# Kernel optimization log

Hardware: AMD Instinct MI355X
Metric: run time of the kernel (lower is better)

The kernel has to match this reference:

```python
import jax, jax.numpy as jnp
import numpy as np

NSAMPLE = 32
EPS = 1e-5


def _fps(xyz, npoint):
    # xyz: [B, N, 3] -> indices [B, npoint] (farthest point sampling, start at idx 0)
    B, N, _ = xyz.shape
    def body(i, state):
        idx, dist, far = state
        idx = idx.at[:, i].set(far)
        centroid = jnp.take_along_axis(xyz, far[:, None, None], axis=1)  # [B,1,3]
        d = jnp.sum((xyz - centroid) ** 2, axis=-1)                      # [B,N]
        dist = jnp.minimum(dist, d)
        far = jnp.argmax(dist, axis=-1).astype(jnp.int32)
        return idx, dist, far
    idx0 = jnp.zeros((B, npoint), jnp.int32)
    dist0 = jnp.full((B, N), 1e10, xyz.dtype)
    far0 = jnp.zeros((B,), jnp.int32)
    idx, _, _ = jax.lax.fori_loop(0, npoint, body, (idx0, dist0, far0))
    return idx


def _knn(query, ref, k):
    # query [B,S,3], ref [B,N,3] -> neighbor idx [B,S,k]
    d = (jnp.sum(query * query, -1)[:, :, None]
         - 2.0 * jnp.einsum('bsc,bnc->bsn', query, ref)
         + jnp.sum(ref * ref, -1)[:, None, :])
    _, idx = jax.lax.top_k(-d, k)
    return idx


def _gather(x, idx):
    # x [B,N,C], idx [B,S,K] -> [B,S,K,C]
    B, S, K = idx.shape
    out = jnp.take_along_axis(x, idx.reshape(B, S * K)[..., None], axis=1)
    return out.reshape(B, S, K, x.shape[-1])


def _set_abstraction(xyz, feat, npoint, weights):
    # xyz [B,N,3], feat [B,N,C]
    fidx = _fps(xyz, npoint)
    new_xyz = jnp.take_along_axis(xyz, fidx[..., None], axis=1)        # [B,S,3]
    nidx = _knn(new_xyz, xyz, NSAMPLE)                                 # [B,S,K]
    g_xyz = _gather(xyz, nidx) - new_xyz[:, :, None, :]                # [B,S,K,3]
    g_feat = _gather(feat, nidx)                                       # [B,S,K,C]
    x = jnp.concatenate([g_xyz, g_feat], axis=-1)                      # [B,S,K,3+C]
    for W in weights:  # 1x1 conv == per-point matmul, then InstanceNorm2d (affine=False) + ReLU
        x = jnp.einsum('bskc,cd->bskd', x, W)
        mu = jnp.mean(x, axis=(1, 2), keepdims=True)
        var = jnp.var(x, axis=(1, 2), keepdims=True)
        x = jax.nn.relu((x - mu) * jax.lax.rsqrt(var + EPS))
    new_feat = jnp.max(x, axis=2)                                      # [B,S,Cout]
    return new_xyz, new_feat, fidx


def setup_inputs() -> dict:
    key = jax.random.key(0)
    ks = jax.random.split(key, 8)
    B, N = 4, 16384
    pc = jax.random.normal(ks[0], (B, 3, N), jnp.float32)
    feature = jax.random.normal(ks[1], (B, 3, N), jnp.float32)
    def w(k, cin, cout):
        return jax.random.normal(k, (cin, cout), jnp.float32) / np.sqrt(cin).astype(np.float32)
    return {
        'pc': pc, 'feature': feature,
        'sa1_w1': w(ks[2], 6, 32),  'sa1_w2': w(ks[3], 32, 32), 'sa1_w3': w(ks[4], 32, 32),
        'sa2_w1': w(ks[5], 35, 64), 'sa2_w2': w(ks[6], 64, 64), 'sa2_w3': w(ks[7], 64, 64),
    }


def reference(pc, feature, sa1_w1, sa1_w2, sa1_w3, sa2_w1, sa2_w2, sa2_w3):
    NPOINT = 4096
    xyz = jnp.transpose(pc, (0, 2, 1))       # [B,N,3]
    feat = jnp.transpose(feature, (0, 2, 1))  # [B,N,3]
    xyz1, feat1, fidx1 = _set_abstraction(xyz, feat, NPOINT // 2, [sa1_w1, sa1_w2, sa1_w3])
    xyz2, feat2, fidx2 = _set_abstraction(xyz1, feat1, NPOINT // 4, [sa2_w1, sa2_w2, sa2_w3])
    # match torch channel-first layout on outputs
    pc_l1 = jnp.transpose(xyz1, (0, 2, 1))
    pc_l2 = jnp.transpose(xyz2, (0, 2, 1))
    feat_l2 = jnp.transpose(feat2, (0, 2, 1))  # [B,64,NPOINT//4]
    return (pc, pc_l1, pc_l2, feat_l2, fidx1, fidx2)
```

## Files before the change

kernel.cpp:

```cpp
#include <hip/hip_runtime.h>
#include <math.h>

namespace {

constexpr int BB = 4;
constexpr int N0 = 16384;
constexpr int S1 = 2048;
constexpr int S2 = 1024;

__device__ __forceinline__ float sq3(float x, float y, float z){
  #pragma clang fp contract(off)
  return x*x + y*y + z*z;
}
__device__ __forceinline__ float sqdist(float ax,float ay,float az,float bx,float by,float bz){
  #pragma clang fp contract(off)
  float dx = ax-bx; float dy = ay-by; float dz = az-bz;
  return dx*dx + dy*dy + dz*dz;
}
__device__ __forceinline__ float dot3(float ax,float ay,float az,float bx,float by,float bz){
  #pragma clang fp contract(off)
  return ax*bx + ay*by + az*bz;
}
__device__ __forceinline__ float knndist(float qs, float dot, float rs){
  #pragma clang fp contract(off)
  return (qs - 2.0f*dot) + rs;
}

__global__ __launch_bounds__(256) void k_setup(const float* __restrict__ pc,
                                               const float* __restrict__ feat,
                                               float* __restrict__ out_pc,
                                               float* __restrict__ xyz,
                                               float* __restrict__ fN,
                                               float* __restrict__ rsq0)
{
  int t = blockIdx.x*256 + threadIdx.x;
  if (t < BB*3*N0) out_pc[t] = pc[t];
  if (t < BB*N0){
    int b = t >> 14, n = t & (N0-1);
    const float* p = pc + (size_t)b*3*N0;
    float x = p[n], y = p[N0+n], z = p[2*N0+n];
    float* q = xyz + (size_t)t*3;
    q[0]=x; q[1]=y; q[2]=z;
    rsq0[t] = sq3(x,y,z);
    const float* f = feat + (size_t)b*3*N0;
    float* g = fN + (size_t)t*3;
    g[0]=f[n]; g[1]=f[N0+n]; g[2]=f[2*N0+n];
  }
}

__device__ __forceinline__ void fps_writeout(int b, int i, float cx, float cy, float cz, int far,
                                             float* sxyz, float* srsq, float* pcl, float* fidxf, int NP)
{
  fidxf[(size_t)b*NP + i] = (float)far;
  float* o = sxyz + ((size_t)b*NP + i)*3;
  o[0]=cx; o[1]=cy; o[2]=cz;
  float* pb = pcl + (size_t)b*3*NP;
  pb[i] = cx; pb[NP+i] = cy; pb[2*NP+i] = cz;
  srsq[(size_t)b*NP + i] = sq3(cx,cy,cz);
}

template<int N, int NP, int BS, int PPT>
__device__ __forceinline__ void fps_body(const float* __restrict__ pts,
                                         float* __restrict__ sxyz,
                                         float* __restrict__ srsq,
                                         float* __restrict__ pcl,
                                         float* __restrict__ fidxf)
{
  static_assert(N == BS*PPT, "bad fps shape");
  constexpr int NW = BS/64;
  int b = blockIdx.x, t = threadIdx.x;
  int lane = t & 63;
  int wid  = t >> 6;
  const float* P = pts + (size_t)b*N*3;

  __shared__ unsigned long long slot[2][NW];

  float px[PPT], py[PPT], pz[PPT], dist[PPT];
  #pragma unroll
  for (int j=0;j<PPT;j++){
    int g = t + BS*j;
    px[j]=P[g*3]; py[j]=P[g*3+1]; pz[j]=P[g*3+2];
    asm volatile("" : "+v"(px[j]), "+v"(py[j]), "+v"(pz[j]));
    dist[j]=1e10f;
  }

  float cx = P[0], cy = P[1], cz = P[2];
  if (t == 0) fps_writeout(b, 0, cx, cy, cz, 0, sxyz, srsq, pcl, fidxf, NP);

  for (int i=1;i<NP;i++){
    int par = i & 1;
    float msq = -1.0f;
    #pragma unroll
    for (int j=0;j<PPT;j++){
      float d  = sqdist(px[j],py[j],pz[j],cx,cy,cz);
      float nd = fminf(dist[j], d);
      dist[j]  = nd;
      msq = fmaxf(msq, nd);
    }
    #pragma unroll
    for (int off=32; off>0; off>>=1) msq = fmaxf(msq, __shfl_xor(msq, off));
    float s = sqrtf(msq);
    unsigned xb = __float_as_uint(msq);
    while (xb > 0u && sqrtf(__uint_as_float(xb - 1u)) == s) xb--;
    float lo = __uint_as_float(xb);
    int li = 0x7FFFFFFF;
    #pragma unroll
    for (int j=PPT-1;j>=0;j--) if (dist[j] >= lo) li = t + BS*j;
    #pragma unroll
    for (int off=32; off>0; off>>=1) li = min(li, __shfl_xor(li, off));
    if (lane == 0)
      slot[par][wid] = ((unsigned long long)__float_as_uint(s) << 32)
                     | (unsigned long long)(unsigned)(~li);
    __syncthreads();
    unsigned long long best = slot[par][0];
    #pragma unroll
    for (int w=1; w<NW; w++){
      unsigned long long o = slot[par][w];
      best = (o > best) ? o : best;
    }
    int far = (int)(~(unsigned)best);
    far = __builtin_amdgcn_readfirstlane(far);
    cx = P[(size_t)far*3]; cy = P[(size_t)far*3+1]; cz = P[(size_t)far*3+2];
    if (t == 0) fps_writeout(b, i, cx, cy, cz, far, sxyz, srsq, pcl, fidxf, NP);
  }
}

__global__ __attribute__((amdgpu_flat_work_group_size(512,512), amdgpu_waves_per_eu(2,2)))
void k_fps1(const float* __restrict__ pts, float* __restrict__ sxyz, float* __restrict__ srsq,
            float* __restrict__ pcl, float* __restrict__ fidxf)
{
  fps_body<N0, S1, 512, 32>(pts, sxyz, srsq, pcl, fidxf);
}

__global__ __attribute__((amdgpu_flat_work_group_size(512,512), amdgpu_waves_per_eu(2,2)))
void k_fps2(const float* __restrict__ pts, float* __restrict__ sxyz, float* __restrict__ srsq,
            float* __restrict__ pcl, float* __restrict__ fidxf)
{
  fps_body<S1, S2, 512, 4>(pts, sxyz, srsq, pcl, fidxf);
}

template<int NREF, int PPT, int NQ>
__global__ __launch_bounds__(512) void k_knn(const float* __restrict__ qxyz,
                                             const float* __restrict__ qrsq,
                                             const float* __restrict__ rxyz,
                                             const float* __restrict__ rrsq,
                                             int* __restrict__ nidx)
{
  static_assert(NREF == 512*PPT, "bad knn shape");
  int q = blockIdx.x;
  int b = q / NQ;
  int t = threadIdx.x;
  const float* R  = rxyz + (size_t)b*NREF*3;
  const float* RS = rrsq + (size_t)b*NREF;
  float qx = qxyz[(size_t)q*3], qy = qxyz[(size_t)q*3+1], qz = qxyz[(size_t)q*3+2];
  float qs = qrsq[q];
  unsigned u[PPT];
  #pragma unroll
  for (int j=0;j<PPT;j++){
    int g = t + 512*j;
    float rx=R[g*3], ry=R[g*3+1], rz=R[g*3+2];
    float d = knndist(qs, dot3(qx,qy,qz,rx,ry,rz), RS[g]);
    unsigned bu = __float_as_uint(d);
    u[j] = ((int)bu < 0) ? ~bu : (bu | 0x80000000u);
  }
  __shared__ unsigned hist[256];
  __shared__ unsigned s_pref, s_pm, s_want, s_cnteq;
  __shared__ int s_n;
  __shared__ int s_eq[1024];
  __shared__ int s_ne;
  if (t == 0){ s_pref=0u; s_pm=0u; s_want=32u; s_n=0; s_ne=0; }

  for (int shift=24; shift>=0; shift-=8){
    if (t < 256) hist[t] = 0u;
    __syncthreads();
    unsigned pref = s_pref, pm = s_pm;
    #pragma unroll
    for (int j=0;j<PPT;j++){
      if ((u[j] & pm) == pref) atomicAdd(&hist[(u[j]>>shift)&255], 1u);
    }
    __syncthreads();
    if (t < 64){
      unsigned h0=hist[4*t], h1=hist[4*t+1], h2=hist[4*t+2], h3=hist[4*t+3];
      unsigned ssum = h0+h1+h2+h3;
      unsigned inc = ssum;
      #pragma unroll
      for (int off=1; off<64; off<<=1){
        unsigned o = __shfl_up(inc, off);
        if (t >= off) inc += o;
      }
      unsigned exc = inc - ssum;
      unsigned want = s_want;
      if (exc < want && want <= inc){
        unsigned rem = want - exc;
        unsigned bin, below;
        if      (rem <= h0)       { bin=4*t+0; below=exc; }
        else if (rem <= h0+h1)    { bin=4*t+1; below=exc+h0; }
        else if (rem <= h0+h1+h2) { bin=4*t+2; below=exc+h0+h1; }
        else                      { bin=4*t+3; below=exc+h0+h1+h2; }
        s_pref = pref | (bin << shift);
        s_pm   = pm   | (0xFFu << shift);
        s_want = want - below;
        if (shift == 0) s_cnteq = hist[bin];
      }
    }
    __syncthreads();
  }
  unsigned T = s_pref;
  unsigned krem = s_want;
  unsigned cnteq = s_cnteq;
  int* outq = nidx + (size_t)q*32;
  #pragma unroll
  for (int j=0;j<PPT;j++){
    if (u[j] < T){ int p = atomicAdd(&s_n, 1); outq[p] = t + 512*j; }
  }
  __syncthreads();
  if (cnteq == krem){
    #pragma unroll
    for (int j=0;j<PPT;j++){
      if (u[j] == T){ int p = atomicAdd(&s_n, 1); outq[p] = t + 512*j; }
    }
  } else {
    #pragma unroll
    for (int j=0;j<PPT;j++){
      if (u[j] == T){ int p = atomicAdd(&s_ne, 1); if (p < 1024) s_eq[p] = t + 512*j; }
    }
    __syncthreads();
    if (t == 0){
      int ne = s_ne; if (ne > 1024) ne = 1024;
      int p = s_n;
      int take = (int)krem; if (take > ne) take = ne;
      for (int r=0; r<take; r++){
        int mn = 0x7FFFFFFF, mi = -1;
        for (int e=0; e<ne; e++){ if (s_eq[e] < mn){ mn = s_eq[e]; mi = e; } }
        if (mi < 0) break;
        outq[p++] = mn;
        s_eq[mi] = 0x7FFFFFFF;
      }
    }
  }
}

template<int C>
__device__ __forceinline__ void accum_sums(const float* o, int b, float* sums){
  __shared__ float s_sum[C];
  __shared__ float s_ssq[C];
  int t = threadIdx.x;
  if (t < C){ s_sum[t]=0.f; s_ssq[t]=0.f; }
  __syncthreads();
  int lane = t & 63;
  #pragma unroll
  for (int c=0;c<C;c++){
    float v = o[c], v2 = v*v;
    #pragma unroll
    for (int off=32; off>0; off>>=1){ v += __shfl_down(v, off); v2 += __shfl_down(v2, off); }
    if (lane == 0){ atomicAdd(&s_sum[c], v); atomicAdd(&s_ssq[c], v2); }
  }
  __syncthreads();
  if (t < C){
    atomicAdd(&sums[(b*64+t)*2],   s_sum[t]);
    atomicAdd(&sums[(b*64+t)*2+1], s_ssq[t]);
  }
}

__global__ __launch_bounds__(256) void k_sa1_l1(const float* __restrict__ xyz,
                                                const float* __restrict__ fN,
                                                const float* __restrict__ sxyz,
                                                const int* __restrict__ nidx,
                                                const float* __restrict__ W,
                                                float* __restrict__ xout,
                                                float* __restrict__ sums)
{
  __shared__ float sW[192];
  int t = threadIdx.x;
  if (t < 192) sW[t] = W[t];
  int row = blockIdx.x*256 + t;
  int b = row >> 16;
  int sk = row & 65535;
  int s = sk >> 5;
  int nb = nidx[row];
  const float* pr = xyz  + ((size_t)(b*N0 + nb))*3;
  const float* pq = sxyz + ((size_t)(b*S1 + s ))*3;
  const float* pf = fN   + ((size_t)(b*N0 + nb))*3;
  float i0 = pr[0]-pq[0], i1 = pr[1]-pq[1], i2 = pr[2]-pq[2];
  float i3 = pf[0], i4 = pf[1], i5 = pf[2];
  __syncthreads();
  float o[32];
  #pragma unroll
  for (int c=0;c<32;c++){
    float a = i0*sW[c];
    a = fmaf(i1, sW[ 32+c], a);
    a = fmaf(i2, sW[ 64+c], a);
    a = fmaf(i3, sW[ 96+c], a);
    a = fmaf(i4, sW[128+c], a);
    a = fmaf(i5, sW[160+c], a);
    o[c] = a;
    xout[(size_t)c*262144 + row] = a;
  }
  accum_sums<32>(o, b, sums);
}

template<int CIN, int COUT, int LRPB>
__global__ __launch_bounds__(256) void k_sa_mid(const float* __restrict__ xin,
                                                const float* __restrict__ W,
                                                const float* __restrict__ sums_in,
                                                float* __restrict__ xout,
                                                float* __restrict__ sums_out,
                                                int rows_total, float invM)
{
  __shared__ float sW[CIN*COUT];
  __shared__ float s_mu[CIN];
  __shared__ float s_rs[CIN];
  int t = threadIdx.x;
  int row = blockIdx.x*256 + t;
  int bb = (blockIdx.x*256) >> LRPB;
  for (int i=t; i<CIN*COUT; i+=256) sW[i] = W[i];
  if (t < CIN){
    float sm = sums_in[(bb*64+t)*2], sq = sums_in[(bb*64+t)*2+1];
    float mu = sm*invM;
    float var = fmaxf(sq*invM - mu*mu, 0.f);
    s_mu[t] = mu;
    s_rs[t] = 1.0f/sqrtf(var + 1e-5f);
  }
  __syncthreads();
  float o[COUT];
  #pragma unroll
  for (int d=0;d<COUT;d++) o[d] = 0.f;
  #pragma unroll
  for (int c=0;c<CIN;c++){
    float x = xin[(size_t)c*rows_total + row];
    float v = fmaxf((x - s_mu[c])*s_rs[c], 0.f);
    #pragma unroll
    for (int d=0;d<COUT;d++) o[d] = fmaf(v, sW[c*COUT+d], o[d]);
  }
  #pragma unroll
  for (int d=0;d<COUT;d++) xout[(size_t)d*rows_total + row] = o[d];
  accum_sums<COUT>(o, bb, sums_out);
}

__global__ __launch_bounds__(256) void k_sa2_l1(const float* __restrict__ xyz1,
                                                const float* __restrict__ feat1,
                                                const float* __restrict__ xyz2,
                                                const int* __restrict__ nidx,
                                                const float* __restrict__ W,
                                                float* __restrict__ xout,
                                                float* __restrict__ sums)
{
  __shared__ float sW[35*64];
  int t = threadIdx.x;
  for (int i=t; i<35*64; i+=256) sW[i] = W[i];
  int row = blockIdx.x*256 + t;
  int b = row >> 15;
  int sk = row & 32767;
  int s = sk >> 5;
  int nb = nidx[row];
  const float* pr = xyz1 + ((size_t)(b*S1 + nb))*3;
  const float* pq = xyz2 + ((size_t)(b*S2 + s ))*3;
  const float* pf = feat1 + ((size_t)(b*S1 + nb))*32;
  float i0 = pr[0]-pq[0], i1 = pr[1]-pq[1], i2 = pr[2]-pq[2];
  float fv[32];
  #pragma unroll
  for (int c=0;c<32;c++) fv[c] = pf[c];
  __syncthreads();
  float o[64];
  #pragma unroll
  for (int d=0;d<64;d++){
    float a = i0*sW[d];
    a = fmaf(i1, sW[ 64+d], a);
    a = fmaf(i2, sW[128+d], a);
    o[d] = a;
  }
  #pragma unroll
  for (int c=0;c<32;c++){
    float v = fv[c];
    #pragma unroll
    for (int d=0;d<64;d++) o[d] = fmaf(v, sW[(3+c)*64+d], o[d]);
  }
  #pragma unroll
  for (int d=0;d<64;d++) xout[(size_t)d*131072 + row] = o[d];
  accum_sums<64>(o, b, sums);
}

template<int C, int PTSB, int CF>
__global__ __launch_bounds__(256) void k_pool(const float* __restrict__ xin,
                                              const float* __restrict__ sums_in,
                                              float* __restrict__ out,
                                              int rows_total, float invM)
{
  int t = threadIdx.x;
  int c = t & (C-1);
  int pl = t / C;
  int p = blockIdx.x*(256/C) + pl;
  int b = p / PTSB;
  float sm = sums_in[(b*64+c)*2], sq = sums_in[(b*64+c)*2+1];
  float mu = sm*invM;
  float var = fmaxf(sq*invM - mu*mu, 0.f);
  float rs = 1.0f/sqrtf(var + 1e-5f);
  const float* xp = xin + (size_t)c*rows_total + (size_t)p*32;
  float m = -1e30f;
  #pragma unroll
  for (int k=0;k<32;k++) m = fmaxf(m, xp[k]);
  m = fmaxf((m - mu)*rs, 0.0f);
  if (CF) out[((size_t)(b*C + c))*PTSB + (p - b*PTSB)] = m;
  else    out[(size_t)p*C + c] = m;
}

constexpr size_t WS_XYZ   = 0;
constexpr size_t WS_FN    = WS_XYZ   + 196608;
constexpr size_t WS_RSQ0  = WS_FN    + 196608;
constexpr size_t WS_XYZ1  = WS_RSQ0  + 65536;
constexpr size_t WS_RSQ1  = WS_XYZ1  + 24576;
constexpr size_t WS_XYZ2  = WS_RSQ1  + 8192;
constexpr size_t WS_RSQ2  = WS_XYZ2  + 12288;
constexpr size_t WS_FEAT1 = WS_RSQ2  + 4096;
constexpr size_t WS_SUMS  = WS_FEAT1 + 262144;
constexpr size_t WS_BUFA  = WS_SUMS  + 3072;
constexpr size_t WS_BUFB  = WS_BUFA  + 8388608;
constexpr size_t WS_NIDX1 = WS_BUFB  + 8388608;
constexpr size_t WS_NIDX2 = WS_NIDX1 + 262144;

constexpr size_t OUT1 = 196608;
constexpr size_t OUT2 = 221184;
constexpr size_t OUT3 = 233472;
constexpr size_t OUT4 = 495616;
constexpr size_t OUT5 = 503808;

}

extern "C" void kernel_launch(void* const* d_in, const int* in_sizes, int n_in,
                              void* d_out, int out_size, void* d_ws, size_t ws_size,
                              hipStream_t stream)
{
  (void)in_sizes; (void)n_in; (void)out_size; (void)ws_size;
  const float* pc   = (const float*)d_in[0];
  const float* feat = (const float*)d_in[1];
  const float* W1 = (const float*)d_in[2];
  const float* W2 = (const float*)d_in[3];
  const float* W3 = (const float*)d_in[4];
  const float* W4 = (const float*)d_in[5];
  const float* W5 = (const float*)d_in[6];
  const float* W6 = (const float*)d_in[7];
  float* out = (float*)d_out;
  float* ws  = (float*)d_ws;

  float* xyz   = ws + WS_XYZ;
  float* fN    = ws + WS_FN;
  float* rsq0  = ws + WS_RSQ0;
  float* xyz1  = ws + WS_XYZ1;
  float* rsq1  = ws + WS_RSQ1;
  float* xyz2  = ws + WS_XYZ2;
  float* rsq2  = ws + WS_RSQ2;
  float* feat1 = ws + WS_FEAT1;
  float* sums  = ws + WS_SUMS;
  float* bufA  = ws + WS_BUFA;
  float* bufB  = ws + WS_BUFB;
  int* nidx1   = (int*)(ws + WS_NIDX1);
  int* nidx2   = (int*)(ws + WS_NIDX2);

  (void)hipMemsetAsync(sums, 0, 3072*sizeof(float), stream);

  k_setup<<<768, 256, 0, stream>>>(pc, feat, out, xyz, fN, rsq0);

  k_fps1<<<BB, 512, 0, stream>>>(xyz, xyz1, rsq1, out+OUT1, out+OUT4);
  k_knn<N0, 32, S1><<<BB*S1, 512, 0, stream>>>(xyz1, rsq1, xyz, rsq0, nidx1);
  k_sa1_l1<<<1024, 256, 0, stream>>>(xyz, fN, xyz1, nidx1, W1, bufA, sums);
  k_sa_mid<32,32,16><<<1024, 256, 0, stream>>>(bufA, W2, sums,       bufB, sums+512,  262144, 1.0f/65536.0f);
  k_sa_mid<32,32,16><<<1024, 256, 0, stream>>>(bufB, W3, sums+512,   bufA, sums+1024, 262144, 1.0f/65536.0f);
  k_pool<32, 2048, 0><<<1024, 256, 0, stream>>>(bufA, sums+1024, feat1, 262144, 1.0f/65536.0f);

  k_fps2<<<BB, 512, 0, stream>>>(xyz1, xyz2, rsq2, out+OUT2, out+OUT5);
  k_knn<S1, 4, S2><<<BB*S2, 512, 0, stream>>>(xyz2, rsq2, xyz1, rsq1, nidx2);
  k_sa2_l1<<<512, 256, 0, stream>>>(xyz1, feat1, xyz2, nidx2, W4, bufB, sums+1536);
  k_sa_mid<64,64,15><<<512, 256, 0, stream>>>(bufB, W5, sums+1536, bufA, sums+2048, 131072, 1.0f/32768.0f);
  k_sa_mid<64,64,15><<<512, 256, 0, stream>>>(bufA, W6, sums+2048, bufB, sums+2560, 131072, 1.0f/32768.0f);
  k_pool<64, 1024, 1><<<1024, 256, 0, stream>>>(bufB, sums+2560, out+OUT3, 131072, 1.0f/32768.0f);
}
```

Baseline: 7.069 ms.

## Move FPS point coordinates to shared memory and double block size

The farthest-point-sampling kernels now keep x/y coordinates (and part of z) in LDS rather than registers, with the rest of z held in registers. This frees enough registers for k_fps1 to run 1024 threads per block with 16 points per thread instead of 512 threads with 32. The aim is to shorten the serial per-iteration scan on the critical path, which runs on only 4 blocks. In exchange, every iteration now does LDS reads and the block-wide reduction covers twice as many waves.

```diff
diff --git a/kernel.cpp b/kernel.cpp
--- a/kernel.cpp
+++ b/kernel.cpp
@@ -59,7 +59,7 @@
   srsq[(size_t)b*NP + i] = sq3(cx,cy,cz);
 }
 
-template<int N, int NP, int BS, int PPT>
+template<int N, int NP, int BS, int PPT, int JZL>
 __device__ __forceinline__ void fps_body(const float* __restrict__ pts,
                                          float* __restrict__ sxyz,
                                          float* __restrict__ srsq,
@@ -67,21 +67,32 @@
                                          float* __restrict__ fidxf)
 {
   static_assert(N == BS*PPT, "bad fps shape");
+  static_assert(JZL <= PPT, "bad JZL");
   constexpr int NW = BS/64;
+  constexpr int ZR = PPT - JZL;
   int b = blockIdx.x, t = threadIdx.x;
   int lane = t & 63;
   int wid  = t >> 6;
   const float* P = pts + (size_t)b*N*3;
 
+  __shared__ float2 s_xy[BS*PPT];
+  __shared__ float  s_z[(JZL > 0 ? JZL : 1)*BS];
   __shared__ unsigned long long slot[2][NW];
 
-  float px[PPT], py[PPT], pz[PPT], dist[PPT];
+  float zr[ZR ? ZR : 1];
+  float dist[PPT];
   #pragma unroll
   for (int j=0;j<PPT;j++){
     int g = t + BS*j;
-    px[j]=P[g*3]; py[j]=P[g*3+1]; pz[j]=P[g*3+2];
-    asm volatile("" : "+v"(px[j]), "+v"(py[j]), "+v"(pz[j]));
-    dist[j]=1e10f;
+    s_xy[g] = make_float2(P[g*3], P[g*3+1]);
+    dist[j] = 1e10f;
+  }
+  #pragma unroll
+  for (int j=0;j<JZL;j++) s_z[t + BS*j] = P[(t + BS*j)*3 + 2];
+  #pragma unroll
+  for (int r=0;r<ZR;r++){
+    zr[r] = P[(size_t)(t + BS*(JZL+r))*3 + 2];
+    asm volatile("" : "+v"(zr[r]));
   }
 
   float cx = P[0], cy = P[1], cz = P[2];
@@ -91,8 +102,18 @@
     int par = i & 1;
     float msq = -1.0f;
     #pragma unroll
-    for (int j=0;j<PPT;j++){
-      float d  = sqdist(px[j],py[j],pz[j],cx,cy,cz);
+    for (int j=0;j<JZL;j++){
+      float2 xy = s_xy[t + BS*j];
+      float d  = sqdist(xy.x, xy.y, s_z[t + BS*j], cx, cy, cz);
+      float nd = fminf(dist[j], d);
+      dist[j]  = nd;
+      msq = fmaxf(msq, nd);
+    }
+    #pragma unroll
+    for (int r=0;r<ZR;r++){
+      int j = JZL + r;
+      float2 xy = s_xy[t + BS*j];
+      float d  = sqdist(xy.x, xy.y, zr[r], cx, cy, cz);
       float nd = fminf(dist[j], d);
       dist[j]  = nd;
       msq = fmaxf(msq, nd);
@@ -125,18 +146,18 @@
   }
 }
 
-__global__ __attribute__((amdgpu_flat_work_group_size(512,512), amdgpu_waves_per_eu(2,2)))
+__global__ __attribute__((amdgpu_flat_work_group_size(1024,1024), amdgpu_waves_per_eu(4,4)))
 void k_fps1(const float* __restrict__ pts, float* __restrict__ sxyz, float* __restrict__ srsq,
             float* __restrict__ pcl, float* __restrict__ fidxf)
 {
-  fps_body<N0, S1, 512, 32>(pts, sxyz, srsq, pcl, fidxf);
+  fps_body<N0, S1, 1024, 16, 7>(pts, sxyz, srsq, pcl, fidxf);
 }
 
 __global__ __attribute__((amdgpu_flat_work_group_size(512,512), amdgpu_waves_per_eu(2,2)))
 void k_fps2(const float* __restrict__ pts, float* __restrict__ sxyz, float* __restrict__ srsq,
             float* __restrict__ pcl, float* __restrict__ fidxf)
 {
-  fps_body<S1, S2, 512, 4>(pts, sxyz, srsq, pcl, fidxf);
+  fps_body<S1, S2, 512, 4, 4>(pts, sxyz, srsq, pcl, fidxf);
 }
 
 template<int NREF, int PPT, int NQ>
@@ -460,7 +481,7 @@
 
   k_setup<<<768, 256, 0, stream>>>(pc, feat, out, xyz, fN, rsq0);
 
-  k_fps1<<<BB, 512, 0, stream>>>(xyz, xyz1, rsq1, out+OUT1, out+OUT4);
+  k_fps1<<<BB, 1024, 0, stream>>>(xyz, xyz1, rsq1, out+OUT1, out+OUT4);
   k_knn<N0, 32, S1><<<BB*S1, 512, 0, stream>>>(xyz1, rsq1, xyz, rsq0, nidx1);
   k_sa1_l1<<<1024, 256, 0, stream>>>(xyz, fN, xyz1, nidx1, W1, bufA, sums);
   k_sa_mid<32,32,16><<<1024, 256, 0, stream>>>(bufA, W2, sums,       bufB, sums+512,  262144, 1.0f/65536.0f);
```

After: 8.629 ms. +22.1%, slower.
